# Kernel optimization log

Hardware: AMD Instinct MI355X
Metric: run time of the kernel (lower is better)

## Reference

```python
import jax, jax.numpy as jnp
import numpy as np

IN_DIM = 96
HIDDEN = 256
EPS = 1e-6
NEG = -1e10


def setup_inputs() -> dict:
    key = jax.random.key(0)
    ks = jax.random.split(key, 12)
    B, S = 8, 2048
    q = jax.random.normal(ks[0], (B, S, IN_DIM), dtype=jnp.float32)
    k = jax.random.normal(ks[1], (B, S, IN_DIM), dtype=jnp.float32)
    v = jax.random.normal(ks[2], (B, S, IN_DIM), dtype=jnp.float32)
    mask = jax.random.randint(ks[3], (B, S, S), 0, 2, dtype=jnp.int32)
    s = 1.0 / np.sqrt(IN_DIM)
    Wq = jax.random.normal(ks[4], (IN_DIM, HIDDEN), dtype=jnp.float32) * s
    bq = jax.random.normal(ks[5], (HIDDEN,), dtype=jnp.float32) * 0.01
    Wk = jax.random.normal(ks[6], (IN_DIM, HIDDEN), dtype=jnp.float32) * s
    bk = jax.random.normal(ks[7], (HIDDEN,), dtype=jnp.float32) * 0.01
    Wv = jax.random.normal(ks[8], (IN_DIM, HIDDEN), dtype=jnp.float32) * s
    bv = jax.random.normal(ks[9], (HIDDEN,), dtype=jnp.float32) * 0.01
    gamma = jnp.ones((HIDDEN,), dtype=jnp.float32)
    beta = jnp.zeros((HIDDEN,), dtype=jnp.float32)
    return {"query": q, "key": k, "value": v, "mask": mask,
            "Wq": Wq, "bq": bq, "Wk": Wk, "bk": bk, "Wv": Wv, "bv": bv,
            "gamma": gamma, "beta": beta}


def reference(query, key, value, mask, Wq, bq, Wk, bk, Wv, bv, gamma, beta):
    # Linear projections: [B,S,96] @ [96,H] -> [B,S,H]
    q = jnp.einsum('bsf,fh->bsh', query, Wq) + bq
    k = jnp.einsum('bsf,fh->bsh', key, Wk) + bk
    v = jnp.einsum('bsf,fh->bsh', value, Wv) + bv
    # Scaled dot-product scores: [B,S,S]
    score = jnp.einsum('bqh,bkh->bqk', q, k) / jnp.sqrt(jnp.float32(HIDDEN))
    score = jnp.where(mask == 0, jnp.float32(NEG), score)
    attn = jax.nn.softmax(score, axis=-1)
    out = jnp.einsum('bqk,bkh->bqh', attn, v)
    # LayerNorm over last dim, eps=1e-6
    mu = jnp.mean(out, axis=-1, keepdims=True)
    var = jnp.mean(jnp.square(out - mu), axis=-1, keepdims=True)
    normed = (out - mu) * jax.lax.rsqrt(var + EPS)
    return normed * gamma + beta
```

## Files before the change

kernel.cpp:

```cpp
#include <hip/hip_runtime.h>

#define B_   8
#define S_   2048
#define IN_  96
#define H_   256
#define NROW (B_ * S_)

typedef float    f32x4 __attribute__((ext_vector_type(4)));
typedef _Float16 f16x8 __attribute__((ext_vector_type(8)));
typedef int      i32x4 __attribute__((ext_vector_type(4)));

__device__ __forceinline__ unsigned short f2h(float x) {
    return __builtin_bit_cast(unsigned short, (_Float16)x);
}
__device__ __forceinline__ float h2f(unsigned short x) {
    return (float)__builtin_bit_cast(_Float16, x);
}
__device__ __forceinline__ void lds_barrier() {
    asm volatile("s_waitcnt lgkmcnt(0)\n\ts_barrier" ::: "memory");
}

__global__ __launch_bounds__(256) void wconv_kernel(
    const float* __restrict__ Wq, const float* __restrict__ Wk,
    const float* __restrict__ Wv, unsigned short* __restrict__ wt)
{
    const int p  = blockIdx.x >> 3;
    const int h0 = (blockIdx.x & 7) * 32;
    const float* W = (p == 0) ? Wq : (p == 1) ? Wk : Wv;
    unsigned short* dst = wt + (size_t)p * H_ * IN_ + (size_t)h0 * IN_;

    __shared__ unsigned short lds[32][100];
    const int t = threadIdx.x;
    #pragma unroll
    for (int i = 0; i < 12; ++i) {
        int idx = i * 256 + t;
        int f = idx >> 5;
        int hl = idx & 31;
        lds[hl][f] = f2h(W[f * H_ + h0 + hl]);
    }
    __syncthreads();
    #pragma unroll
    for (int j = 0; j < 6; ++j) {
        int e = (j * 256 + t) * 2;
        int hl = e / IN_, f = e % IN_;
        unsigned int pk = (unsigned int)lds[hl][f] |
                          ((unsigned int)lds[hl][f + 1] << 16);
        ((unsigned int*)dst)[j * 256 + t] = pk;
    }
}

__global__ __launch_bounds__(256) void maskpack_kernel(
    const int* __restrict__ mask, unsigned* __restrict__ pm32)
{
    __shared__ unsigned char nib[4][8][64];
    const int wave = threadIdx.x >> 6;
    const int lane = threadIdx.x & 63;
    const int wid  = blockIdx.x * 4 + wave;
    const int r0   = wid * 2;

    const int* m0 = mask + (size_t)r0 * S_ + lane * 4;
    const int* m1 = m0 + S_;
    i32x4 a[8], b[8];
    #pragma unroll
    for (int j = 0; j < 8; ++j)
        a[j] = __builtin_nontemporal_load((const i32x4*)(m0 + j * 256));
    #pragma unroll
    for (int j = 0; j < 8; ++j)
        b[j] = __builtin_nontemporal_load((const i32x4*)(m1 + j * 256));

    #pragma unroll
    for (int j = 0; j < 8; ++j) {
        unsigned n0 = (a[j][0] != 0 ? 1u : 0u) | (a[j][1] != 0 ? 2u : 0u)
                    | (a[j][2] != 0 ? 4u : 0u) | (a[j][3] != 0 ? 8u : 0u);
        unsigned n1 = (b[j][0] != 0 ? 1u : 0u) | (b[j][1] != 0 ? 2u : 0u)
                    | (b[j][2] != 0 ? 4u : 0u) | (b[j][3] != 0 ? 8u : 0u);
        nib[wave][j][lane] = (unsigned char)(n0 | (n1 << 4));
    }
    asm volatile("s_waitcnt lgkmcnt(0)" ::: "memory");

    unsigned long long v = *(const unsigned long long*)
        &nib[wave][lane >> 3][(lane & 7) * 8];
    unsigned long long x0 = v & 0x0F0F0F0F0F0F0F0FULL;
    unsigned long long x1 = (v >> 4) & 0x0F0F0F0F0F0F0F0FULL;
    x0 = (x0 | (x0 >> 4))  & 0x00FF00FF00FF00FFULL;
    x1 = (x1 | (x1 >> 4))  & 0x00FF00FF00FF00FFULL;
    x0 = (x0 | (x0 >> 8))  & 0x0000FFFF0000FFFFULL;
    x1 = (x1 | (x1 >> 8))  & 0x0000FFFF0000FFFFULL;
    x0 = (x0 | (x0 >> 16)) & 0xFFFFFFFFULL;
    x1 = (x1 | (x1 >> 16)) & 0xFFFFFFFFULL;

    pm32[(size_t)r0 * 64 + lane]       = (unsigned)x0;
    pm32[(size_t)(r0 + 1) * 64 + lane] = (unsigned)x1;
}

__global__ __launch_bounds__(256) void proj_kernel3(
    const float* __restrict__ query, const float* __restrict__ key,
    const float* __restrict__ value, const unsigned short* __restrict__ wt,
    const float* __restrict__ bq, const float* __restrict__ bk,
    const float* __restrict__ bv,
    unsigned short* __restrict__ pq, unsigned short* __restrict__ pk,
    unsigned short* __restrict__ pv)
{
    __shared__ unsigned short Xs[3][16][104];

    const int t    = threadIdx.x;
    const int lane = t & 63;
    const int wave = t >> 6;
    const int col  = lane & 15;
    const int quad = lane >> 4;
    const int bi   = blockIdx.x;
    const int s0   = bi * 16;
    const int b    = s0 >> 11;
    const int sl   = s0 & (S_ - 1);

    const float* srcs[3] = { query + (size_t)s0 * IN_,
                             key   + (size_t)s0 * IN_,
                             value + (size_t)s0 * IN_ };
    #pragma unroll
    for (int p = 0; p < 3; ++p) {
        #pragma unroll
        for (int i = 0; i < 2; ++i) {
            int idx = i * 256 + t;
            if (idx < 384) {
                f32x4 x = *(const f32x4*)(srcs[p] + idx * 4);
                int r = idx / 24;
                int f = (idx - r * 24) * 4;
                unsigned long long pkk =
                    (unsigned long long)f2h(x[0])
                  | ((unsigned long long)f2h(x[1]) << 16)
                  | ((unsigned long long)f2h(x[2]) << 32)
                  | ((unsigned long long)f2h(x[3]) << 48);
                *(unsigned long long*)&Xs[p][r][f] = pkk;
            }
        }
    }
    __syncthreads();

    const int hc = wave;
    #pragma unroll
    for (int p = 0; p < 3; ++p) {
        const unsigned short* wbase = wt + (size_t)p * H_ * IN_;
        f16x8 wfr[4][3];
        #pragma unroll
        for (int ht = 0; ht < 4; ++ht)
            #pragma unroll
            for (int kc = 0; kc < 3; ++kc)
                wfr[ht][kc] = *(const f16x8*)(wbase
                    + (size_t)(hc * 64 + ht * 16 + col) * IN_ + kc * 32 + quad * 8);
        f16x8 xfr[3];
        #pragma unroll
        for (int kc = 0; kc < 3; ++kc)
            xfr[kc] = *(const f16x8*)&Xs[p][col][kc * 32 + quad * 8];

        f32x4 acc[4];
        #pragma unroll
        for (int ht = 0; ht < 4; ++ht) acc[ht] = (f32x4)(0.0f);
        #pragma unroll
        for (int kc = 0; kc < 3; ++kc)
            #pragma unroll
            for (int ht = 0; ht < 4; ++ht)
                acc[ht] = (p < 2)
                    ? __builtin_amdgcn_mfma_f32_16x16x32_f16(xfr[kc], wfr[ht][kc], acc[ht], 0, 0, 0)
                    : __builtin_amdgcn_mfma_f32_16x16x32_f16(wfr[ht][kc], xfr[kc], acc[ht], 0, 0, 0);

        if (p < 2) {
            unsigned short* dst  = (p == 0) ? pq : pk;
            const float*    bias = (p == 0) ? bq : bk;
            #pragma unroll
            for (int ht = 0; ht < 4; ++ht) {
                float bh = bias[hc * 64 + ht * 16 + col];
                const int s    = hc * 2 + (ht >> 1);
                const int lq   = ((ht & 1) * 2 + (col >> 3)) * 16;
                const int j    = col & 7;
                #pragma unroll
                for (int r = 0; r < 4; ++r)
                    dst[(size_t)(((bi * 8 + s) * 64 + lq + quad * 4 + r)) * 8 + j]
                        = f2h(acc[ht][r] + bh);
            }
        } else {
            const int kl  = (sl & 63) + col;
            const int c   = sl >> 6;
            const int s2  = kl >> 5;
            const int qv  = (kl >> 3) & 3;
            const int jj  = col & 7;
            #pragma unroll
            for (int ht = 0; ht < 4; ++ht) {
                f32x4 b4 = *(const f32x4*)(bv + hc * 64 + ht * 16 + quad * 4);
                #pragma unroll
                for (int r = 0; r < 4; ++r)
                    pv[(size_t)(((b * 32 + c) * 32 + hc * 8 + ht * 2 + s2) * 64
                                + qv * 16 + quad * 4 + r) * 8 + jj]
                        = f2h(acc[ht][r] + b4[r]);
            }
        }
    }
}

__global__ __launch_bounds__(256, 3) void attn_kernel(
    const unsigned short* __restrict__ pq, const unsigned short* __restrict__ pk,
    const unsigned short* __restrict__ pv, const unsigned long long* __restrict__ pm,
    unsigned short* __restrict__ Opart, float* __restrict__ lpart)
{
    __shared__ __align__(16) unsigned short Qs[8192];
    __shared__ unsigned short P[2][32][68];
    __shared__ float lsum[4][32];

    const int tid  = threadIdx.x;
    const int wave = tid >> 6;
    const int lane = tid & 63;
    const int col  = lane & 15;
    const int quad = lane >> 4;

    const int b     = blockIdx.x & 7;
    const int strip = (blockIdx.x >> 3) & 63;
    const int kh    = blockIdx.x >> 9;
    const int q0    = strip << 5;

    {
        const unsigned short* qsrc = pq + (size_t)(b * 128 + strip * 2) * 4096;
        #pragma unroll
        for (int ph = 0; ph < 4; ++ph) {
            int i = ph * 2048 + tid * 8;
            *(f16x8*)&Qs[i] = *(const f16x8*)(qsrc + i);
        }
    }

    f32x4 O[2][4];
    #pragma unroll
    for (int st = 0; st < 2; ++st)
        #pragma unroll
        for (int ht = 0; ht < 4; ++ht) O[st][ht] = (f32x4)(0.0f);
    float l0 = 0.0f, l1 = 0.0f;

    const unsigned short* pkb = pk + (size_t)(b * 128) * 4096 + lane * 8;
    const unsigned short* pvb = pv + (size_t)(b * 32) * 32 * 512
                                   + (size_t)wave * 8 * 512 + lane * 8;

    const unsigned* pm32 = (const unsigned*)pm;
    const int sh = (wave & 1) * 16 + quad * 4;
    const unsigned* mp0 = pm32 + (size_t)(b * S_ + q0 + col) * 64
                        + kh * 16 + (wave >> 1);
    const unsigned* mp1 = mp0 + 16 * 64;

    f16x8 kf[8];
    #pragma unroll
    for (int s = 0; s < 8; ++s)
        kf[s] = *(const f16x8*)(pkb + (size_t)(kh * 32 + wave) * 4096 + s * 512);

    unsigned mc0 = mp0[0];
    unsigned mc1 = mp1[0];

    lds_barrier();

    {
        f32x4 St0 = (f32x4)(0.0f), St1 = (f32x4)(0.0f);
        __builtin_amdgcn_s_setprio(1);
        #pragma unroll
        for (int s = 0; s < 8; ++s) {
            f16x8 q0f = *(const f16x8*)&Qs[s * 512 + lane * 8];
            f16x8 q1f = *(const f16x8*)&Qs[4096 + s * 512 + lane * 8];
            St0 = __builtin_amdgcn_mfma_f32_16x16x32_f16(kf[s], q0f, St0, 0, 0, 0);
            St1 = __builtin_amdgcn_mfma_f32_16x16x32_f16(kf[s], q1f, St1, 0, 0, 0);
        }
        __builtin_amdgcn_s_setprio(0);

        {
            const unsigned short* kb = pkb + (size_t)(kh * 32 + 4 + wave) * 4096;
            #pragma unroll
            for (int s = 0; s < 8; ++s)
                kf[s] = *(const f16x8*)(kb + s * 512);
        }
        unsigned mn0 = mp0[2];
        unsigned mn1 = mp1[2];

        {
            unsigned bits = mc0 >> sh;
            unsigned long long pk64 = 0;
            #pragma unroll
            for (int r = 0; r < 4; ++r) {
                float e = exp2f(fmaf(St0[r], 0.0901679843f, -8.65617025f));
                float p = ((bits >> r) & 1u) ? e : 0.0f;
                _Float16 ph = (_Float16)p;
                l0 += (float)ph;
                pk64 |= (unsigned long long)__builtin_bit_cast(unsigned short, ph)
                        << (16 * r);
            }
            *(unsigned long long*)&P[0][col][wave * 16 + quad * 4] = pk64;
        }
        {
            unsigned bits = mc1 >> sh;
            unsigned long long pk64 = 0;
            #pragma unroll
            for (int r = 0; r < 4; ++r) {
                float e = exp2f(fmaf(St1[r], 0.0901679843f, -8.65617025f));
                float p = ((bits >> r) & 1u) ? e : 0.0f;
                _Float16 ph = (_Float16)p;
                l1 += (float)ph;
                pk64 |= (unsigned long long)__builtin_bit_cast(unsigned short, ph)
                        << (16 * r);
            }
            *(unsigned long long*)&P[0][16 + col][wave * 16 + quad * 4] = pk64;
        }
        mc0 = mn0; mc1 = mn1;

        lds_barrier();
    }

    #pragma unroll 2
    for (int i = 0; i < 7; ++i) {
        const int pb  = i & 1;
        const int cn2 = (i < 5) ? i + 2 : 7;
        const int gc  = kh * 8 + i;

        const unsigned short* vb = pvb + (size_t)gc * 32 * 512;
        f16x8 vf[4][2];
        #pragma unroll
        for (int ht = 0; ht < 4; ++ht)
            #pragma unroll
            for (int s2 = 0; s2 < 2; ++s2)
                vf[ht][s2] = *(const f16x8*)(vb + (size_t)(ht * 2 + s2) * 512);

        f32x4 St0 = (f32x4)(0.0f), St1 = (f32x4)(0.0f);
        __builtin_amdgcn_s_setprio(1);
        #pragma unroll
        for (int s = 0; s < 8; ++s) {
            f16x8 q0f = *(const f16x8*)&Qs[s * 512 + lane * 8];
            f16x8 q1f = *(const f16x8*)&Qs[4096 + s * 512 + lane * 8];
            St0 = __builtin_amdgcn_mfma_f32_16x16x32_f16(kf[s], q0f, St0, 0, 0, 0);
            St1 = __builtin_amdgcn_mfma_f32_16x16x32_f16(kf[s], q1f, St1, 0, 0, 0);
        }
        __builtin_amdgcn_s_setprio(0);

        {
            const unsigned short* kb = pkb + (size_t)(kh * 32 + cn2 * 4 + wave) * 4096;
            #pragma unroll
            for (int s = 0; s < 8; ++s)
                kf[s] = *(const f16x8*)(kb + s * 512);
        }
        unsigned mn0 = mp0[cn2 * 2];
        unsigned mn1 = mp1[cn2 * 2];

        {
            unsigned bits = mc0 >> sh;
            unsigned long long pk64 = 0;
            #pragma unroll
            for (int r = 0; r < 4; ++r) {
                float e = exp2f(fmaf(St0[r], 0.0901679843f, -8.65617025f));
                float p = ((bits >> r) & 1u) ? e : 0.0f;
                _Float16 ph = (_Float16)p;
                l0 += (float)ph;
                pk64 |= (unsigned long long)__builtin_bit_cast(unsigned short, ph)
                        << (16 * r);
            }
            *(unsigned long long*)&P[pb ^ 1][col][wave * 16 + quad * 4] = pk64;
        }
        {
            unsigned bits = mc1 >> sh;
            unsigned long long pk64 = 0;
            #pragma unroll
            for (int r = 0; r < 4; ++r) {
                float e = exp2f(fmaf(St1[r], 0.0901679843f, -8.65617025f));
                float p = ((bits >> r) & 1u) ? e : 0.0f;
                _Float16 ph = (_Float16)p;
                l1 += (float)ph;
                pk64 |= (unsigned long long)__builtin_bit_cast(unsigned short, ph)
                        << (16 * r);
            }
            *(unsigned long long*)&P[pb ^ 1][16 + col][wave * 16 + quad * 4] = pk64;
        }
        mc0 = mn0; mc1 = mn1;

        __builtin_amdgcn_s_setprio(1);
        #pragma unroll
        for (int st = 0; st < 2; ++st) {
            #pragma unroll
            for (int s2 = 0; s2 < 2; ++s2) {
                union { unsigned long long u[2]; f16x8 v; } pu;
                const unsigned short* pr = &P[pb][st * 16 + col][s2 * 32 + quad * 8];
                pu.u[0] = *(const unsigned long long*)pr;
                pu.u[1] = *(const unsigned long long*)(pr + 4);
                f16x8 pf = pu.v;
                #pragma unroll
                for (int ht = 0; ht < 4; ++ht)
                    O[st][ht] = __builtin_amdgcn_mfma_f32_16x16x32_f16(pf, vf[ht][s2], O[st][ht], 0, 0, 0);
            }
        }
        __builtin_amdgcn_s_setprio(0);

        lds_barrier();
    }

    {
        const unsigned short* vb = pvb + (size_t)(kh * 8 + 7) * 32 * 512;
        f16x8 vf[4][2];
        #pragma unroll
        for (int ht = 0; ht < 4; ++ht)
            #pragma unroll
            for (int s2 = 0; s2 < 2; ++s2)
                vf[ht][s2] = *(const f16x8*)(vb + (size_t)(ht * 2 + s2) * 512);
        __builtin_amdgcn_s_setprio(1);
        #pragma unroll
        for (int st = 0; st < 2; ++st) {
            #pragma unroll
            for (int s2 = 0; s2 < 2; ++s2) {
                union { unsigned long long u[2]; f16x8 v; } pu;
                const unsigned short* pr = &P[1][st * 16 + col][s2 * 32 + quad * 8];
                pu.u[0] = *(const unsigned long long*)pr;
                pu.u[1] = *(const unsigned long long*)(pr + 4);
                f16x8 pf = pu.v;
                #pragma unroll
                for (int ht = 0; ht < 4; ++ht)
                    O[st][ht] = __builtin_amdgcn_mfma_f32_16x16x32_f16(pf, vf[ht][s2], O[st][ht], 0, 0, 0);
            }
        }
        __builtin_amdgcn_s_setprio(0);
    }

    l0 += __shfl_xor(l0, 16); l0 += __shfl_xor(l0, 32);
    l1 += __shfl_xor(l1, 16); l1 += __shfl_xor(l1, 32);
    if (lane < 16) { lsum[wave][lane] = l0; lsum[wave][16 + lane] = l1; }
    __syncthreads();

    if (wave == 0 && lane < 16) {
        #pragma unroll
        for (int st = 0; st < 2; ++st) {
            float lt = lsum[0][st * 16 + lane] + lsum[1][st * 16 + lane]
                     + lsum[2][st * 16 + lane] + lsum[3][st * 16 + lane];
            lpart[(size_t)kh * NROW + b * S_ + q0 + st * 16 + lane] = lt;
        }
    }

    unsigned short* OT = Qs;
    #pragma unroll
    for (int st = 0; st < 2; ++st)
        #pragma unroll
        for (int ht = 0; ht < 4; ++ht)
            #pragma unroll
            for (int r = 0; r < 4; ++r)
                OT[(st * 16 + quad * 4 + r) * 256 + wave * 64 + ht * 16 + col]
                    = f2h(O[st][ht][r]);
    __syncthreads();

    unsigned short* ob = Opart + (size_t)kh * NROW * H_
                       + (size_t)(b * S_ + q0) * H_;
    const int r8 = tid >> 5;
    const int c8 = (tid & 31) * 8;
    #pragma unroll
    for (int j = 0; j < 4; ++j) {
        const int row = j * 8 + r8;
        *(f16x8*)(ob + (size_t)row * H_ + c8)
            = *(const f16x8*)(OT + row * 256 + c8);
    }
}

__global__ __launch_bounds__(256) void merge_ln_kernel(
    const unsigned short* __restrict__ Opart, const float* __restrict__ lpart,
    const float* __restrict__ gamma, const float* __restrict__ beta,
    float* __restrict__ out)
{
    const int row  = blockIdx.x * 4 + (threadIdx.x >> 6);
    const int lane = threadIdx.x & 63;

    float linv = 1.0f / (lpart[row] + lpart[NROW + row]
                       + lpart[2 * NROW + row] + lpart[3 * NROW + row]);

    const unsigned short* o0 = Opart + (size_t)row * H_ + lane * 4;
    unsigned long long a0 = *(const unsigned long long*)o0;
    unsigned long long a1 = *(const unsigned long long*)(o0 + (size_t)NROW * H_);
    unsigned long long a2 = *(const unsigned long long*)(o0 + (size_t)2 * NROW * H_);
    unsigned long long a3 = *(const unsigned long long*)(o0 + (size_t)3 * NROW * H_);

    float vals[4];
    float sum = 0.0f;
    #pragma unroll
    for (int j = 0; j < 4; ++j) {
        vals[j] = (h2f((unsigned short)(a0 >> (16 * j)))
                 + h2f((unsigned short)(a1 >> (16 * j)))
                 + h2f((unsigned short)(a2 >> (16 * j)))
                 + h2f((unsigned short)(a3 >> (16 * j)))) * linv;
        sum += vals[j];
    }
    sum += __shfl_xor(sum, 1);  sum += __shfl_xor(sum, 2);
    sum += __shfl_xor(sum, 4);  sum += __shfl_xor(sum, 8);
    sum += __shfl_xor(sum, 16); sum += __shfl_xor(sum, 32);
    float mu = sum * (1.0f / H_);

    float sq = 0.0f;
    #pragma unroll
    for (int j = 0; j < 4; ++j) {
        float d = vals[j] - mu;
        sq += d * d;
    }
    sq += __shfl_xor(sq, 1);  sq += __shfl_xor(sq, 2);
    sq += __shfl_xor(sq, 4);  sq += __shfl_xor(sq, 8);
    sq += __shfl_xor(sq, 16); sq += __shfl_xor(sq, 32);
    float rstd = rsqrtf(sq * (1.0f / H_) + 1e-6f);

    f32x4 g  = *(const f32x4*)(gamma + lane * 4);
    f32x4 be = *(const f32x4*)(beta  + lane * 4);
    f32x4 o;
    #pragma unroll
    for (int j = 0; j < 4; ++j)
        o[j] = (vals[j] - mu) * rstd * g[j] + be[j];
    *(f32x4*)(out + (size_t)row * H_ + lane * 4) = o;
}

extern "C" void kernel_launch(void* const* d_in, const int* in_sizes, int n_in,
                              void* d_out, int out_size, void* d_ws, size_t ws_size,
                              hipStream_t stream)
{
    const float* query = (const float*)d_in[0];
    const float* key   = (const float*)d_in[1];
    const float* value = (const float*)d_in[2];
    const int*   mask  = (const int*)d_in[3];
    const float* Wq = (const float*)d_in[4];
    const float* bq = (const float*)d_in[5];
    const float* Wk = (const float*)d_in[6];
    const float* bk = (const float*)d_in[7];
    const float* Wv = (const float*)d_in[8];
    const float* bv = (const float*)d_in[9];
    const float* gamma = (const float*)d_in[10];
    const float* beta  = (const float*)d_in[11];
    float* out = (float*)d_out;

    const size_t NQK = (size_t)B_ * S_ * H_;
    unsigned short* pq = (unsigned short*)d_ws;
    unsigned short* pk = pq + NQK;
    unsigned short* pv = pk + NQK;
    unsigned short* wt = pv + NQK;
    unsigned short* Op = wt + (size_t)3 * H_ * IN_;
    float*          lp = (float*)(Op + (size_t)4 * NROW * H_);
    unsigned long long* pm = (unsigned long long*)(lp + 4 * NROW);

    wconv_kernel<<<24, 256, 0, stream>>>(Wq, Wk, Wv, wt);
    maskpack_kernel<<<2048, 256, 0, stream>>>(mask, (unsigned*)pm);
    proj_kernel3<<<B_ * S_ / 16, 256, 0, stream>>>(query, key, value, wt,
                                                   bq, bk, bv, pq, pk, pv);
    attn_kernel<<<B_ * S_ / 32 * 4, 256, 0, stream>>>(pq, pk, pv, pm, Op, lp);
    merge_ln_kernel<<<NROW / 4, 256, 0, stream>>>(Op, lp, gamma, beta, out);
}
```

Before: 307.0 us.

## Fuse mask packing into projection and LayerNorm into attention; drop key split

Mask packing now runs inside the projection kernel: every third block packs mask rows while the others do projections, and one launch replaces two. The attention kernel no longer splits keys into four parts. Each block walks all key chunks for its 32-row strip and applies normalization and LayerNorm in-kernel from a padded LDS tile, so the separate merge kernel and the fp16 partial-output round trip are removed. In exchange the attention grid shrinks from 2048 to 512 blocks, which cuts parallelism and may leave CUs underused, and each block runs a four-times-longer serial loop.

```diff
diff --git a/kernel.cpp b/kernel.cpp
--- a/kernel.cpp
+++ b/kernel.cpp
@@ -49,66 +49,68 @@
     }
 }
 
-__global__ __launch_bounds__(256) void maskpack_kernel(
-    const int* __restrict__ mask, unsigned* __restrict__ pm32)
-{
-    __shared__ unsigned char nib[4][8][64];
-    const int wave = threadIdx.x >> 6;
-    const int lane = threadIdx.x & 63;
-    const int wid  = blockIdx.x * 4 + wave;
-    const int r0   = wid * 2;
-
-    const int* m0 = mask + (size_t)r0 * S_ + lane * 4;
-    const int* m1 = m0 + S_;
-    i32x4 a[8], b[8];
-    #pragma unroll
-    for (int j = 0; j < 8; ++j)
-        a[j] = __builtin_nontemporal_load((const i32x4*)(m0 + j * 256));
-    #pragma unroll
-    for (int j = 0; j < 8; ++j)
-        b[j] = __builtin_nontemporal_load((const i32x4*)(m1 + j * 256));
-
-    #pragma unroll
-    for (int j = 0; j < 8; ++j) {
-        unsigned n0 = (a[j][0] != 0 ? 1u : 0u) | (a[j][1] != 0 ? 2u : 0u)
-                    | (a[j][2] != 0 ? 4u : 0u) | (a[j][3] != 0 ? 8u : 0u);
-        unsigned n1 = (b[j][0] != 0 ? 1u : 0u) | (b[j][1] != 0 ? 2u : 0u)
-                    | (b[j][2] != 0 ? 4u : 0u) | (b[j][3] != 0 ? 8u : 0u);
-        nib[wave][j][lane] = (unsigned char)(n0 | (n1 << 4));
-    }
-    asm volatile("s_waitcnt lgkmcnt(0)" ::: "memory");
-
-    unsigned long long v = *(const unsigned long long*)
-        &nib[wave][lane >> 3][(lane & 7) * 8];
-    unsigned long long x0 = v & 0x0F0F0F0F0F0F0F0FULL;
-    unsigned long long x1 = (v >> 4) & 0x0F0F0F0F0F0F0F0FULL;
-    x0 = (x0 | (x0 >> 4))  & 0x00FF00FF00FF00FFULL;
-    x1 = (x1 | (x1 >> 4))  & 0x00FF00FF00FF00FFULL;
-    x0 = (x0 | (x0 >> 8))  & 0x0000FFFF0000FFFFULL;
-    x1 = (x1 | (x1 >> 8))  & 0x0000FFFF0000FFFFULL;
-    x0 = (x0 | (x0 >> 16)) & 0xFFFFFFFFULL;
-    x1 = (x1 | (x1 >> 16)) & 0xFFFFFFFFULL;
-
-    pm32[(size_t)r0 * 64 + lane]       = (unsigned)x0;
-    pm32[(size_t)(r0 + 1) * 64 + lane] = (unsigned)x1;
-}
-
-__global__ __launch_bounds__(256) void proj_kernel3(
+__global__ __launch_bounds__(256) void projmask_kernel(
     const float* __restrict__ query, const float* __restrict__ key,
     const float* __restrict__ value, const unsigned short* __restrict__ wt,
     const float* __restrict__ bq, const float* __restrict__ bk,
-    const float* __restrict__ bv,
+    const float* __restrict__ bv, const int* __restrict__ mask,
     unsigned short* __restrict__ pq, unsigned short* __restrict__ pk,
-    unsigned short* __restrict__ pv)
+    unsigned short* __restrict__ pv, unsigned* __restrict__ pm32)
 {
     __shared__ unsigned short Xs[3][16][104];
+    __shared__ unsigned char nib[4][8][64];
+
+    const int bid = blockIdx.x;
+    if ((bid % 3) == 2) {
+        const int wave = threadIdx.x >> 6;
+        const int lane = threadIdx.x & 63;
+        const int wid  = (bid / 3) * 4 + wave;
+        #pragma unroll
+        for (int rr = 0; rr < 4; ++rr) {
+            const int r0 = wid * 8 + rr * 2;
+            const int* m0 = mask + (size_t)r0 * S_ + lane * 4;
+            const int* m1 = m0 + S_;
+            i32x4 a[8], b[8];
+            #pragma unroll
+            for (int j = 0; j < 8; ++j)
+                a[j] = __builtin_nontemporal_load((const i32x4*)(m0 + j * 256));
+            #pragma unroll
+            for (int j = 0; j < 8; ++j)
+                b[j] = __builtin_nontemporal_load((const i32x4*)(m1 + j * 256));
+
+            #pragma unroll
+            for (int j = 0; j < 8; ++j) {
+                unsigned n0 = (a[j][0] != 0 ? 1u : 0u) | (a[j][1] != 0 ? 2u : 0u)
+                            | (a[j][2] != 0 ? 4u : 0u) | (a[j][3] != 0 ? 8u : 0u);
+                unsigned n1 = (b[j][0] != 0 ? 1u : 0u) | (b[j][1] != 0 ? 2u : 0u)
+                            | (b[j][2] != 0 ? 4u : 0u) | (b[j][3] != 0 ? 8u : 0u);
+                nib[wave][j][lane] = (unsigned char)(n0 | (n1 << 4));
+            }
+            asm volatile("s_waitcnt lgkmcnt(0)" ::: "memory");
+
+            unsigned long long v = *(const unsigned long long*)
+                &nib[wave][lane >> 3][(lane & 7) * 8];
+            unsigned long long x0 = v & 0x0F0F0F0F0F0F0F0FULL;
+            unsigned long long x1 = (v >> 4) & 0x0F0F0F0F0F0F0F0FULL;
+            x0 = (x0 | (x0 >> 4))  & 0x00FF00FF00FF00FFULL;
+            x1 = (x1 | (x1 >> 4))  & 0x00FF00FF00FF00FFULL;
+            x0 = (x0 | (x0 >> 8))  & 0x0000FFFF0000FFFFULL;
+            x1 = (x1 | (x1 >> 8))  & 0x0000FFFF0000FFFFULL;
+            x0 = (x0 | (x0 >> 16)) & 0xFFFFFFFFULL;
+            x1 = (x1 | (x1 >> 16)) & 0xFFFFFFFFULL;
+
+            pm32[(size_t)r0 * 64 + lane]       = (unsigned)x0;
+            pm32[(size_t)(r0 + 1) * 64 + lane] = (unsigned)x1;
+        }
+        return;
+    }
+    const int bi = (bid / 3) * 2 + (bid % 3);
 
     const int t    = threadIdx.x;
     const int lane = t & 63;
     const int wave = t >> 6;
     const int col  = lane & 15;
     const int quad = lane >> 4;
-    const int bi   = blockIdx.x;
     const int s0   = bi * 16;
     const int b    = s0 >> 11;
     const int sl   = s0 & (S_ - 1);
@@ -199,11 +201,13 @@
 __global__ __launch_bounds__(256, 3) void attn_kernel(
     const unsigned short* __restrict__ pq, const unsigned short* __restrict__ pk,
     const unsigned short* __restrict__ pv, const unsigned long long* __restrict__ pm,
-    unsigned short* __restrict__ Opart, float* __restrict__ lpart)
+    const float* __restrict__ gamma, const float* __restrict__ beta,
+    float* __restrict__ out)
 {
-    __shared__ __align__(16) unsigned short Qs[8192];
+    __shared__ __align__(16) unsigned short Qs[8448];
     __shared__ unsigned short P[2][32][68];
     __shared__ float lsum[4][32];
+    __shared__ float linv_s[32];
 
     const int tid  = threadIdx.x;
     const int wave = tid >> 6;
@@ -212,8 +216,7 @@
     const int quad = lane >> 4;
 
     const int b     = blockIdx.x & 7;
-    const int strip = (blockIdx.x >> 3) & 63;
-    const int kh    = blockIdx.x >> 9;
+    const int strip = blockIdx.x >> 3;
     const int q0    = strip << 5;
 
     {
@@ -238,14 +241,13 @@
 
     const unsigned* pm32 = (const unsigned*)pm;
     const int sh = (wave & 1) * 16 + quad * 4;
-    const unsigned* mp0 = pm32 + (size_t)(b * S_ + q0 + col) * 64
-                        + kh * 16 + (wave >> 1);
+    const unsigned* mp0 = pm32 + (size_t)(b * S_ + q0 + col) * 64 + (wave >> 1);
     const unsigned* mp1 = mp0 + 16 * 64;
 
     f16x8 kf[8];
     #pragma unroll
     for (int s = 0; s < 8; ++s)
-        kf[s] = *(const f16x8*)(pkb + (size_t)(kh * 32 + wave) * 4096 + s * 512);
+        kf[s] = *(const f16x8*)(pkb + (size_t)wave * 4096 + s * 512);
 
     unsigned mc0 = mp0[0];
     unsigned mc1 = mp1[0];
@@ -265,7 +267,7 @@
         __builtin_amdgcn_s_setprio(0);
 
         {
-            const unsigned short* kb = pkb + (size_t)(kh * 32 + 4 + wave) * 4096;
+            const unsigned short* kb = pkb + (size_t)(4 + wave) * 4096;
             #pragma unroll
             for (int s = 0; s < 8; ++s)
                 kf[s] = *(const f16x8*)(kb + s * 512);
@@ -307,12 +309,11 @@
     }
 
     #pragma unroll 2
-    for (int i = 0; i < 7; ++i) {
+    for (int i = 0; i < 31; ++i) {
         const int pb  = i & 1;
-        const int cn2 = (i < 5) ? i + 2 : 7;
-        const int gc  = kh * 8 + i;
-
-        const unsigned short* vb = pvb + (size_t)gc * 32 * 512;
+        const int cn2 = (i < 29) ? i + 2 : 31;
+
+        const unsigned short* vb = pvb + (size_t)i * 32 * 512;
         f16x8 vf[4][2];
         #pragma unroll
         for (int ht = 0; ht < 4; ++ht)
@@ -332,7 +333,7 @@
         __builtin_amdgcn_s_setprio(0);
 
         {
-            const unsigned short* kb = pkb + (size_t)(kh * 32 + cn2 * 4 + wave) * 4096;
+            const unsigned short* kb = pkb + (size_t)(cn2 * 4 + wave) * 4096;
             #pragma unroll
             for (int s = 0; s < 8; ++s)
                 kf[s] = *(const f16x8*)(kb + s * 512);
@@ -391,7 +392,7 @@
     }
 
     {
-        const unsigned short* vb = pvb + (size_t)(kh * 8 + 7) * 32 * 512;
+        const unsigned short* vb = pvb + (size_t)31 * 32 * 512;
         f16x8 vf[4][2];
         #pragma unroll
         for (int ht = 0; ht < 4; ++ht)
@@ -421,13 +422,9 @@
     if (lane < 16) { lsum[wave][lane] = l0; lsum[wave][16 + lane] = l1; }
     __syncthreads();
 
-    if (wave == 0 && lane < 16) {
-        #pragma unroll
-        for (int st = 0; st < 2; ++st) {
-            float lt = lsum[0][st * 16 + lane] + lsum[1][st * 16 + lane]
-                     + lsum[2][st * 16 + lane] + lsum[3][st * 16 + lane];
-            lpart[(size_t)kh * NROW + b * S_ + q0 + st * 16 + lane] = lt;
-        }
+    if (tid < 32) {
+        float lt = lsum[0][tid] + lsum[1][tid] + lsum[2][tid] + lsum[3][tid];
+        linv_s[tid] = 1.0f / lt;
     }
 
     unsigned short* OT = Qs;
@@ -437,72 +434,47 @@
         for (int ht = 0; ht < 4; ++ht)
             #pragma unroll
             for (int r = 0; r < 4; ++r)
-                OT[(st * 16 + quad * 4 + r) * 256 + wave * 64 + ht * 16 + col]
+                OT[(st * 16 + quad * 4 + r) * 264 + wave * 64 + ht * 16 + col]
                     = f2h(O[st][ht][r]);
     __syncthreads();
 
-    unsigned short* ob = Opart + (size_t)kh * NROW * H_
-                       + (size_t)(b * S_ + q0) * H_;
-    const int r8 = tid >> 5;
-    const int c8 = (tid & 31) * 8;
-    #pragma unroll
-    for (int j = 0; j < 4; ++j) {
-        const int row = j * 8 + r8;
-        *(f16x8*)(ob + (size_t)row * H_ + c8)
-            = *(const f16x8*)(OT + row * 256 + c8);
-    }
-}
-
-__global__ __launch_bounds__(256) void merge_ln_kernel(
-    const unsigned short* __restrict__ Opart, const float* __restrict__ lpart,
-    const float* __restrict__ gamma, const float* __restrict__ beta,
-    float* __restrict__ out)
-{
-    const int row  = blockIdx.x * 4 + (threadIdx.x >> 6);
-    const int lane = threadIdx.x & 63;
-
-    float linv = 1.0f / (lpart[row] + lpart[NROW + row]
-                       + lpart[2 * NROW + row] + lpart[3 * NROW + row]);
-
-    const unsigned short* o0 = Opart + (size_t)row * H_ + lane * 4;
-    unsigned long long a0 = *(const unsigned long long*)o0;
-    unsigned long long a1 = *(const unsigned long long*)(o0 + (size_t)NROW * H_);
-    unsigned long long a2 = *(const unsigned long long*)(o0 + (size_t)2 * NROW * H_);
-    unsigned long long a3 = *(const unsigned long long*)(o0 + (size_t)3 * NROW * H_);
-
-    float vals[4];
-    float sum = 0.0f;
-    #pragma unroll
-    for (int j = 0; j < 4; ++j) {
-        vals[j] = (h2f((unsigned short)(a0 >> (16 * j)))
-                 + h2f((unsigned short)(a1 >> (16 * j)))
-                 + h2f((unsigned short)(a2 >> (16 * j)))
-                 + h2f((unsigned short)(a3 >> (16 * j)))) * linv;
-        sum += vals[j];
-    }
-    sum += __shfl_xor(sum, 1);  sum += __shfl_xor(sum, 2);
-    sum += __shfl_xor(sum, 4);  sum += __shfl_xor(sum, 8);
-    sum += __shfl_xor(sum, 16); sum += __shfl_xor(sum, 32);
-    float mu = sum * (1.0f / H_);
-
-    float sq = 0.0f;
-    #pragma unroll
-    for (int j = 0; j < 4; ++j) {
-        float d = vals[j] - mu;
-        sq += d * d;
-    }
-    sq += __shfl_xor(sq, 1);  sq += __shfl_xor(sq, 2);
-    sq += __shfl_xor(sq, 4);  sq += __shfl_xor(sq, 8);
-    sq += __shfl_xor(sq, 16); sq += __shfl_xor(sq, 32);
-    float rstd = rsqrtf(sq * (1.0f / H_) + 1e-6f);
-
     f32x4 g  = *(const f32x4*)(gamma + lane * 4);
     f32x4 be = *(const f32x4*)(beta  + lane * 4);
-    f32x4 o;
-    #pragma unroll
-    for (int j = 0; j < 4; ++j)
-        o[j] = (vals[j] - mu) * rstd * g[j] + be[j];
-    *(f32x4*)(out + (size_t)row * H_ + lane * 4) = o;
+    #pragma unroll
+    for (int p = 0; p < 8; ++p) {
+        const int row = p * 4 + wave;
+        float linv = linv_s[row];
+        unsigned long long a =
+            *(const unsigned long long*)&OT[row * 264 + lane * 4];
+        float vals[4];
+        float sum = 0.0f;
+        #pragma unroll
+        for (int j = 0; j < 4; ++j) {
+            vals[j] = h2f((unsigned short)(a >> (16 * j))) * linv;
+            sum += vals[j];
+        }
+        sum += __shfl_xor(sum, 1);  sum += __shfl_xor(sum, 2);
+        sum += __shfl_xor(sum, 4);  sum += __shfl_xor(sum, 8);
+        sum += __shfl_xor(sum, 16); sum += __shfl_xor(sum, 32);
+        float mu = sum * (1.0f / H_);
+
+        float sq = 0.0f;
+        #pragma unroll
+        for (int j = 0; j < 4; ++j) {
+            float d = vals[j] - mu;
+            sq += d * d;
+        }
+        sq += __shfl_xor(sq, 1);  sq += __shfl_xor(sq, 2);
+        sq += __shfl_xor(sq, 4);  sq += __shfl_xor(sq, 8);
+        sq += __shfl_xor(sq, 16); sq += __shfl_xor(sq, 32);
+        float rstd = rsqrtf(sq * (1.0f / H_) + 1e-6f);
+
+        f32x4 o;
+        #pragma unroll
+        for (int j = 0; j < 4; ++j)
+            o[j] = (vals[j] - mu) * rstd * g[j] + be[j];
+        *(f32x4*)(out + (size_t)(b * S_ + q0 + row) * H_ + lane * 4) = o;
+    }
 }
 
 extern "C" void kernel_launch(void* const* d_in, const int* in_sizes, int n_in,
@@ -528,14 +500,12 @@
     unsigned short* pk = pq + NQK;
     unsigned short* pv = pk + NQK;
     unsigned short* wt = pv + NQK;
-    unsigned short* Op = wt + (size_t)3 * H_ * IN_;
-    float*          lp = (float*)(Op + (size_t)4 * NROW * H_);
-    unsigned long long* pm = (unsigned long long*)(lp + 4 * NROW);
+    unsigned long long* pm = (unsigned long long*)
+        (wt + (size_t)3 * H_ * IN_);
 
     wconv_kernel<<<24, 256, 0, stream>>>(Wq, Wk, Wv, wt);
-    maskpack_kernel<<<2048, 256, 0, stream>>>(mask, (unsigned*)pm);
-    proj_kernel3<<<B_ * S_ / 16, 256, 0, stream>>>(query, key, value, wt,
-                                                   bq, bk, bv, pq, pk, pv);
-    attn_kernel<<<B_ * S_ / 32 * 4, 256, 0, stream>>>(pq, pk, pv, pm, Op, lp);
-    merge_ln_kernel<<<NROW / 4, 256, 0, stream>>>(Op, lp, gamma, beta, out);
-}
+    projmask_kernel<<<1536, 256, 0, stream>>>(query, key, value, wt,
+                                              bq, bk, bv, mask,
+                                              pq, pk, pv, (unsigned*)pm);
+    attn_kernel<<<512, 256, 0, stream>>>(pq, pk, pv, pm, gamma, beta, out);
+}
```

After: 291.5 us (median of 2 runs). -5.0%, faster.
